# Optimization experiments

Hardware: AMD Instinct MI355X
Metric: run time of the kernel (lower is better)

## Reference

```python
import jax, jax.numpy as jnp
import numpy as np

IN_FEATURES = 2048
OUT_FEATURES = 8192


def setup_inputs() -> dict:
    key = jax.random.key(0)
    k_x, k_w, k_s, k_b = jax.random.split(key, 4)
    x = jax.random.normal(k_x, (4, 2048, IN_FEATURES), dtype=jnp.float32)
    # int8 weights as produced by quantize(): values in [-128, 127]
    weight_int8 = jax.random.randint(k_w, (OUT_FEATURES, IN_FEATURES), -128, 128, dtype=jnp.int8)
    # per-output-row scale, shape [out_features, 1]
    scale = jax.random.uniform(k_s, (OUT_FEATURES, 1), dtype=jnp.float32, minval=1e-4, maxval=0.02)
    bias = jax.random.normal(k_b, (OUT_FEATURES,), dtype=jnp.float32) * 0.01
    return {"x": x, "weight_int8": weight_int8, "scale": scale, "bias": bias}


def reference(x, weight_int8, scale, bias):
    # dequantize: [out, in] int8 -> x.dtype, scaled per output row
    weight = weight_int8.astype(x.dtype) * scale.astype(x.dtype)
    # F.linear: x @ weight.T + bias
    return jnp.einsum('bsi,oi->bso', x, weight) + bias.astype(x.dtype)
```

## Files before the change

### kernel.cpp

```cpp
#include <hip/hip_runtime.h>
#include <hip/hip_bf16.h>

#define M_DIM 8192
#define N_DIM 8192
#define K_DIM 2048

#define BK 64
#define NT (K_DIM / BK)
#define SLOT_BYTES 16384

typedef float f32x4 __attribute__((ext_vector_type(4)));
typedef int   i32x4 __attribute__((ext_vector_type(4)));
typedef unsigned int u32;
typedef u32 u32x2 __attribute__((ext_vector_type(2)));
typedef u32 u32x4 __attribute__((ext_vector_type(4)));


__device__ __forceinline__ void gload16(const unsigned char* g, char* l) {
    __builtin_amdgcn_global_load_lds(
        (const __attribute__((address_space(1))) u32*)g,
        (__attribute__((address_space(3))) u32*)l, 16, 0, 0);
}

__device__ __forceinline__ u32 pack4(int a, int b, int c, int d) {
    return (u32)(a & 255) | ((u32)(b & 255) << 8) |
           ((u32)(c & 255) << 16) | ((u32)(d & 255) << 24);
}


__global__ void __launch_bounds__(256) quant_x_k(const float* __restrict__ x,
                                                 unsigned char* __restrict__ xq,
                                                 float* __restrict__ sx) {
    const int row = blockIdx.x;
    const int t = threadIdx.x;
    const float* xr = x + (size_t)row * K_DIM;
    f32x4 v0 = *((const f32x4*)xr + t * 2);
    f32x4 v1 = *((const f32x4*)xr + t * 2 + 1);
    float m = fabsf(v0[0]);
    m = fmaxf(m, fabsf(v0[1])); m = fmaxf(m, fabsf(v0[2])); m = fmaxf(m, fabsf(v0[3]));
    m = fmaxf(m, fabsf(v1[0])); m = fmaxf(m, fabsf(v1[1]));
    m = fmaxf(m, fabsf(v1[2])); m = fmaxf(m, fabsf(v1[3]));
#pragma unroll
    for (int off = 32; off >= 1; off >>= 1)
        m = fmaxf(m, __shfl_xor(m, off, 64));
    __shared__ float wmax[4];
    if ((t & 63) == 0) wmax[t >> 6] = m;
    __syncthreads();
    m = fmaxf(fmaxf(wmax[0], wmax[1]), fmaxf(wmax[2], wmax[3]));
    m = fmaxf(m, 1e-20f);
    const float rs = 127.0f / m;
    u32x2 o;
    o[0] = pack4((int)rintf(v0[0] * rs), (int)rintf(v0[1] * rs),
                 (int)rintf(v0[2] * rs), (int)rintf(v0[3] * rs));
    o[1] = pack4((int)rintf(v1[0] * rs), (int)rintf(v1[1] * rs),
                 (int)rintf(v1[2] * rs), (int)rintf(v1[3] * rs));
    *((u32x2*)(xq + (size_t)row * K_DIM) + t) = o;
    if (t == 0) sx[row] = m / 127.0f;
}


__global__ void __launch_bounds__(256) cvt_w_k(const int* __restrict__ w,
                                               unsigned char* __restrict__ Bt) {
    const int g = blockIdx.x;
    const int t = threadIdx.x;
    const int fr = t >> 4;
    const int kc = t & 15;
    const int col = g * 16 + fr;
    const int* wr = w + (size_t)col * K_DIM + kc * 128;

#pragma unroll
    for (int kk = 0; kk < 8; ++kk) {
        const int k = kc * 128 + kk * 16;
        const int kt = k >> 6;
        const int s4 = (k >> 4) & 3;
        u32x4 o;
#pragma unroll
        for (int j = 0; j < 4; ++j) {
            i32x4 a = *(const i32x4*)(wr + kk * 16 + j * 4);
            o[j] = pack4(a[0], a[1], a[2], a[3]);
        }
        *(u32x4*)(Bt + (size_t)g * 32768 + kt * 1024 + (s4 * 16 + fr) * 16) = o;
    }
}


__global__ void __launch_bounds__(512, 2)
gemm_i8(const unsigned char* __restrict__ Aq, const unsigned char* __restrict__ Bt,
        const float* __restrict__ sx, const float* __restrict__ sw,
        const float* __restrict__ bias, float* __restrict__ C) {
    extern __shared__ __align__(16) char ldsb[];

    const int bid = blockIdx.x;
    const int swz = (bid & 7) * 128 + (bid >> 3);
    const int rowBase = (swz >> 5) * 256;
    const int colBase = (swz & 31) * 256;

    const int t = threadIdx.x;
    const int l = t & 63;
    const int w = t >> 6;
    const int wm = w >> 2;
    const int wn = w & 3;
    const int fr = l & 15;
    const int s4 = l >> 4;

    const int sr = t >> 2;
    const int sk = (((t & 3) ^ ((sr >> 1) & 3)) * 16);
    const unsigned char* gA0 = Aq + (size_t)(rowBase + sr) * K_DIM + sk;
    const unsigned char* gA1 = Aq + (size_t)(rowBase + 128 + sr) * K_DIM + sk;

#define STAGE_A(tk) do { \
        char* _b = ldsb + ((tk) & 3) * SLOT_BYTES; \
        const int _k = (tk) * BK; \
        gload16(gA0 + _k, _b + t * 16); \
        gload16(gA1 + _k, _b + 8192 + t * 16); \
    } while (0)

    const unsigned char* bB[4];
#pragma unroll
    for (int ni = 0; ni < 4; ++ni)
        bB[ni] = Bt + (size_t)(colBase / 16 + wn * 4 + ni) * 32768 + l * 16;

#define BLOAD(dst, T) do { \
        _Pragma("unroll") \
        for (int ni = 0; ni < 4; ++ni) \
            dst[ni] = *(const i32x4*)(bB[ni] + (T) * 1024); \
    } while (0)

    const int pc = ((s4 ^ ((fr >> 1) & 3)) * 16);
    int aoff[8];
#pragma unroll
    for (int mi = 0; mi < 8; ++mi)
        aoff[mi] = (wm * 128 + mi * 16 + fr) * 64 + pc;

    i32x4 acc[8][4] = {};
    i32x4 afC[8], bf0[4], bf1[4];

#define SB    __builtin_amdgcn_sched_barrier(0)
#define BAR   __builtin_amdgcn_s_barrier()
#define P1    __builtin_amdgcn_s_setprio(1)
#define P0p   __builtin_amdgcn_s_setprio(0)
#define LGKM0 asm volatile("s_waitcnt lgkmcnt(0)" ::: "memory")
#define VM6   asm volatile("s_waitcnt vmcnt(6)" ::: "memory")
#define VM4   asm volatile("s_waitcnt vmcnt(4)" ::: "memory")
#define VM0   asm volatile("s_waitcnt vmcnt(0)" ::: "memory")

#define READS_A(tk) do { \
        const char* _s = ldsb + ((tk) & 3) * SLOT_BYTES; \
        _Pragma("unroll") \
        for (int mi = 0; mi < 8; ++mi) afC[mi] = *(const i32x4*)(_s + aoff[mi]); \
    } while (0)

#define MFMA_ILV(BREG, NTK) do { P1; \
        const char* _n = ldsb + ((NTK) & 3) * SLOT_BYTES; \
        _Pragma("unroll") \
        for (int mi = 0; mi < 8; ++mi) { \
            _Pragma("unroll") \
            for (int ni = 0; ni < 4; ++ni) \
                acc[mi][ni] = __builtin_amdgcn_mfma_i32_16x16x64_i8( \
                    afC[mi], BREG[ni], acc[mi][ni], 0, 0, 0); \
            afC[mi] = *(const i32x4*)(_n + aoff[mi]); \
        } \
        P0p; } while (0)

#define MFMA_ALL(BREG) do { P1; \
        _Pragma("unroll") \
        for (int mi = 0; mi < 8; ++mi) \
            _Pragma("unroll") \
            for (int ni = 0; ni < 4; ++ni) \
                acc[mi][ni] = __builtin_amdgcn_mfma_i32_16x16x64_i8( \
                    afC[mi], BREG[ni], acc[mi][ni], 0, 0, 0); \
        P0p; } while (0)

#define BODY(T, BCUR, BNXT, DOSTG, VMW) do { \
        BLOAD(BNXT, (T) + 1); \
        if (DOSTG) STAGE_A((T) + 3); \
        VMW; LGKM0; SB; BAR; SB; \
        MFMA_ILV(BCUR, (T) + 1); \
    } while (0)

    STAGE_A(0); STAGE_A(1); STAGE_A(2);
    BLOAD(bf0, 0);
    VM4; SB; BAR; SB;
    READS_A(0);

    BODY(0, bf0, bf1, true, VM6);
#pragma unroll 1
    for (int T = 1; T <= 27; T += 2) {
        BODY(T,     bf1, bf0, true, VM6);
        BODY(T + 1, bf0, bf1, true, VM6);
    }
    BODY(29, bf1, bf0, false, VM6);
    BODY(30, bf0, bf1, false, VM4);
    VM0; LGKM0; SB;
    MFMA_ALL(bf1);

#undef BODY
#undef MFMA_ALL
#undef MFMA_ILV
#undef READS_A
#undef BLOAD
#undef STAGE_A

#pragma unroll
    for (int ni = 0; ni < 4; ++ni) {
        const int col = colBase + wn * 64 + ni * 16 + fr;
        const float swc = sw[col];
        const float bz = bias[col];
#pragma unroll
        for (int mi = 0; mi < 8; ++mi) {
            const int rb = rowBase + wm * 128 + mi * 16 + s4 * 4;
            i32x4 a = acc[mi][ni];
#pragma unroll
            for (int r = 0; r < 4; ++r)
                C[(size_t)(rb + r) * N_DIM + col] =
                    (float)a[r] * (sx[rb + r] * swc) + bz;
        }
    }
}


typedef int i32x4_t __attribute__((ext_vector_type(4)));
__global__ void __launch_bounds__(256) naive_k(const float* __restrict__ x,
                                               const int* __restrict__ w,
                                               const float* __restrict__ scale,
                                               const float* __restrict__ bias,
                                               float* __restrict__ out) {
    __shared__ float xs[K_DIM];
    const int m = blockIdx.x >> 5;
    const int n = ((blockIdx.x & 31) << 8) + threadIdx.x;
    for (int i = threadIdx.x; i < K_DIM; i += 256) xs[i] = x[(size_t)m * K_DIM + i];
    __syncthreads();
    const int* wr = w + (size_t)n * K_DIM;
    float acc = 0.f;
    for (int k = 0; k < K_DIM; k += 4) {
        i32x4_t v = *(const i32x4_t*)(wr + k);
        acc += xs[k]     * (float)v[0];
        acc += xs[k + 1] * (float)v[1];
        acc += xs[k + 2] * (float)v[2];
        acc += xs[k + 3] * (float)v[3];
    }
    out[(size_t)m * N_DIM + n] = acc * scale[n] + bias[n];
}


extern "C" void kernel_launch(void* const* d_in, const int* in_sizes, int n_in,
                              void* d_out, int out_size, void* d_ws, size_t ws_size,
                              hipStream_t stream) {
    const float* x     = (const float*)d_in[0];
    const int*   w8    = (const int*)d_in[1];
    const float* sw    = (const float*)d_in[2];
    const float* bias  = (const float*)d_in[3];
    float*       out   = (float*)d_out;

    const size_t xq_bytes = (size_t)M_DIM * K_DIM;
    const size_t wq_bytes = (size_t)N_DIM * K_DIM;
    const size_t need = xq_bytes + wq_bytes + (size_t)M_DIM * sizeof(float);
    if (ws_size >= need) {
        unsigned char* xq = (unsigned char*)d_ws;
        unsigned char* Bt = xq + xq_bytes;
        float* sx = (float*)(Bt + wq_bytes);
        hipFuncSetAttribute((const void*)gemm_i8,
                            hipFuncAttributeMaxDynamicSharedMemorySize, 65536);
        quant_x_k<<<M_DIM, 256, 0, stream>>>(x, xq, sx);
        cvt_w_k<<<N_DIM / 16, 256, 0, stream>>>(w8, Bt);
        gemm_i8<<<dim3((M_DIM / 256) * (N_DIM / 256)), 512, 65536, stream>>>(
            xq, Bt, sx, sw, bias, out);
    } else {
        naive_k<<<(M_DIM * (N_DIM / 256)), 256, 0, stream>>>(x, w8, sw, bias, out);
    }
}
```

Measured before the change: 218.9 us.

## Deepen A-tile LDS ring to five slots and double B prefetch distance

New measurement: 204.1 us, median of 5. 1.07x faster.

```diff
diff --git a/kernel.cpp b/kernel.cpp
--- a/kernel.cpp
+++ b/kernel.cpp
@@ -109,7 +109,7 @@
     const unsigned char* gA1 = Aq + (size_t)(rowBase + 128 + sr) * K_DIM + sk;
 
 #define STAGE_A(tk) do { \
-        char* _b = ldsb + ((tk) & 3) * SLOT_BYTES; \
+        char* _b = ldsb + ((tk) % 5) * SLOT_BYTES; \
         const int _k = (tk) * BK; \
         gload16(gA0 + _k, _b + t * 16); \
         gload16(gA1 + _k, _b + 8192 + t * 16); \
@@ -135,23 +135,22 @@
     i32x4 acc[8][4] = {};
     i32x4 afC[8], bf0[4], bf1[4];
 
-#define SB    __builtin_amdgcn_sched_barrier(0)
+#define SBF   __builtin_amdgcn_sched_barrier(0)
 #define BAR   __builtin_amdgcn_s_barrier()
-#define P1    __builtin_amdgcn_s_setprio(1)
-#define P0p   __builtin_amdgcn_s_setprio(0)
 #define LGKM0 asm volatile("s_waitcnt lgkmcnt(0)" ::: "memory")
-#define VM6   asm volatile("s_waitcnt vmcnt(6)" ::: "memory")
+#define VM12  asm volatile("s_waitcnt vmcnt(12)" ::: "memory")
+#define VM8   asm volatile("s_waitcnt vmcnt(8)" ::: "memory")
 #define VM4   asm volatile("s_waitcnt vmcnt(4)" ::: "memory")
 #define VM0   asm volatile("s_waitcnt vmcnt(0)" ::: "memory")
 
-#define READS_A(tk) do { \
-        const char* _s = ldsb + ((tk) & 3) * SLOT_BYTES; \
+#define READS_A(slot) do { \
+        const char* _s = ldsb + (slot) * SLOT_BYTES; \
         _Pragma("unroll") \
         for (int mi = 0; mi < 8; ++mi) afC[mi] = *(const i32x4*)(_s + aoff[mi]); \
     } while (0)
 
-#define MFMA_ILV(BREG, NTK) do { P1; \
-        const char* _n = ldsb + ((NTK) & 3) * SLOT_BYTES; \
+#define MFMA_ILV(BREG, NSLOT) do { \
+        const char* _n = ldsb + (NSLOT) * SLOT_BYTES; \
         _Pragma("unroll") \
         for (int mi = 0; mi < 8; ++mi) { \
             _Pragma("unroll") \
@@ -160,41 +159,45 @@
                     afC[mi], BREG[ni], acc[mi][ni], 0, 0, 0); \
             afC[mi] = *(const i32x4*)(_n + aoff[mi]); \
         } \
-        P0p; } while (0)
-
-#define MFMA_ALL(BREG) do { P1; \
+    } while (0)
+
+#define MFMA_ALL(BREG) do { \
         _Pragma("unroll") \
         for (int mi = 0; mi < 8; ++mi) \
             _Pragma("unroll") \
             for (int ni = 0; ni < 4; ++ni) \
                 acc[mi][ni] = __builtin_amdgcn_mfma_i32_16x16x64_i8( \
                     afC[mi], BREG[ni], acc[mi][ni], 0, 0, 0); \
-        P0p; } while (0)
-
-#define BODY(T, BCUR, BNXT, DOSTG, VMW) do { \
-        BLOAD(BNXT, (T) + 1); \
-        if (DOSTG) STAGE_A((T) + 3); \
-        VMW; LGKM0; SB; BAR; SB; \
-        MFMA_ILV(BCUR, (T) + 1); \
-    } while (0)
-
-    STAGE_A(0); STAGE_A(1); STAGE_A(2);
-    BLOAD(bf0, 0);
-    VM4; SB; BAR; SB;
+    } while (0)
+
+#define SBODY(T, DOSTG, VMMID) do { \
+        VM4; LGKM0; SBF; BAR; SBF; \
+        if (DOSTG) { STAGE_A((T) + 4); STAGE_A((T) + 5); } \
+        MFMA_ILV(bf0, ((T) + 1) % 5); \
+        BLOAD(bf0, (T) + 2); \
+        VMMID; LGKM0; SBF; \
+        MFMA_ILV(bf1, ((T) + 2) % 5); \
+        BLOAD(bf1, (T) + 3); \
+    } while (0)
+
+    STAGE_A(0); STAGE_A(1); STAGE_A(2); STAGE_A(3);
+    BLOAD(bf0, 0); BLOAD(bf1, 1);
+    VM12; SBF; BAR; SBF;
     READS_A(0);
 
-    BODY(0, bf0, bf1, true, VM6);
-#pragma unroll 1
-    for (int T = 1; T <= 27; T += 2) {
-        BODY(T,     bf1, bf0, true, VM6);
-        BODY(T + 1, bf0, bf1, true, VM6);
-    }
-    BODY(29, bf1, bf0, false, VM6);
-    BODY(30, bf0, bf1, false, VM4);
-    VM0; LGKM0; SB;
+    SBODY(0,  true, VM8);  SBODY(2,  true, VM8);  SBODY(4,  true, VM8);
+    SBODY(6,  true, VM8);  SBODY(8,  true, VM8);  SBODY(10, true, VM8);
+    SBODY(12, true, VM8);  SBODY(14, true, VM8);  SBODY(16, true, VM8);
+    SBODY(18, true, VM8);  SBODY(20, true, VM8);  SBODY(22, true, VM8);
+    SBODY(24, true, VM8);  SBODY(26, true, VM8);
+    SBODY(28, false, VM4);
+
+    VM4; LGKM0; SBF;
+    MFMA_ILV(bf0, 31 % 5);
+    VM0; LGKM0; SBF;
     MFMA_ALL(bf1);
 
-#undef BODY
+#undef SBODY
 #undef MFMA_ALL
 #undef MFMA_ILV
 #undef READS_A
@@ -260,10 +263,10 @@
         unsigned char* Bt = xq + xq_bytes;
         float* sx = (float*)(Bt + wq_bytes);
         hipFuncSetAttribute((const void*)gemm_i8,
-                            hipFuncAttributeMaxDynamicSharedMemorySize, 65536);
+                            hipFuncAttributeMaxDynamicSharedMemorySize, 5 * SLOT_BYTES);
         quant_x_k<<<M_DIM, 256, 0, stream>>>(x, xq, sx);
         cvt_w_k<<<N_DIM / 16, 256, 0, stream>>>(w8, Bt);
-        gemm_i8<<<dim3((M_DIM / 256) * (N_DIM / 256)), 512, 65536, stream>>>(
+        gemm_i8<<<dim3((M_DIM / 256) * (N_DIM / 256)), 512, 5 * SLOT_BYTES, stream>>>(
             xq, Bt, sx, sw, bias, out);
     } else {
         naive_k<<<(M_DIM * (N_DIM / 256)), 256, 0, stream>>>(x, w8, sw, bias, out);
```
